# Kernel tuning notes

Hardware: AMD Instinct MI355X
Metric: run time of the kernel (lower is better)

The kernel has to match this reference:

```python
import jax, jax.numpy as jnp
import numpy as np

B_SZ, L, D_MODEL = 2, 1024, 1024
D_INNER, D_STATE, D_CONV = 2048, 16, 4
EPS = 1e-6


def setup_inputs() -> dict:
    key = jax.random.key(0)
    ks = jax.random.split(key, 8)
    def n(k, shape, scale=0.02):
        return jax.random.normal(k, shape, jnp.float32) * scale
    return {
        "x": jax.random.normal(ks[0], (B_SZ, L, D_MODEL), jnp.float32),
        "W_in": n(ks[1], (D_MODEL, 2 * D_INNER)),
        "b_in": jnp.zeros((2 * D_INNER,), jnp.float32),
        "conv_w": n(ks[2], (D_INNER, 1, D_CONV), 0.2),
        "conv_b": jnp.zeros((D_INNER,), jnp.float32),
        "W_xp": n(ks[3], (D_INNER, 2 * D_STATE)),
        "b_xp": jnp.zeros((2 * D_STATE,), jnp.float32),
        "W_dt": n(ks[4], (D_INNER, D_INNER)),
        "b_dt": jnp.full((D_INNER,), -1.0, jnp.float32),
        # torch code does log(randn) (NaN-prone); use log of positive uniform instead
        "A_log": jnp.log(jax.random.uniform(ks[5], (D_INNER, D_STATE), jnp.float32, 0.5, 1.5)),
        "D_skip": jnp.ones((D_INNER,), jnp.float32),
        "W_out": n(ks[6], (D_INNER, D_MODEL)),
        "b_out": jnp.zeros((D_MODEL,), jnp.float32),
        "alpha": jnp.ones((D_MODEL,), jnp.float32),
        "beta": jnp.zeros((D_MODEL,), jnp.float32),
    }


def _selective_scan(xc, delta, A, Bm, Cm, D_skip):
    # xc, delta: (B,L,di); A: (di,ds); Bm, Cm: (B,L,ds)
    dA = jnp.exp(delta[..., None] * A)                     # (B,L,di,ds)
    dBx = (delta * xc)[..., None] * Bm[:, :, None, :]      # (B,L,di,ds)
    h0 = jnp.zeros((xc.shape[0], xc.shape[2], A.shape[1]), xc.dtype)

    def step(h, inp):
        dA_t, dBx_t, C_t = inp
        h = dA_t * h + dBx_t                               # (B,di,ds)
        y_t = jnp.einsum('bds,bs->bd', h, C_t)
        return h, y_t

    _, ys = jax.lax.scan(
        step, h0,
        (dA.transpose(1, 0, 2, 3), dBx.transpose(1, 0, 2, 3), Cm.transpose(1, 0, 2)))
    y = ys.transpose(1, 0, 2)                              # (B,L,di)
    return y + D_skip * xc


def _layernorm(r, alpha, beta):
    # torch LayerNormalization: unbiased std, eps added to std
    mean = jnp.mean(r, axis=-1, keepdims=True)
    diff = r - mean
    var_unb = jnp.sum(diff * diff, axis=-1, keepdims=True) / (r.shape[-1] - 1)
    std = jnp.sqrt(var_unb)
    return alpha * diff / (std + EPS) + beta


def reference(x, W_in, b_in, conv_w, conv_b, W_xp, b_xp, W_dt, b_dt,
              A_log, D_skip, W_out, b_out, alpha, beta):
    residual = x
    xz = x @ W_in + b_in                                   # (B,L,2*di)
    x_in, z = jnp.split(xz, 2, axis=-1)

    # depthwise causal conv1d (torch pads d_conv-1 both sides, slices [:L])
    xt = x_in.transpose(0, 2, 1)                           # (B,di,L)
    xt = jax.lax.conv_general_dilated(
        xt, conv_w, window_strides=(1,), padding=[(D_CONV - 1, 0)],
        feature_group_count=D_INNER, dimension_numbers=('NCH', 'OIH', 'NCH'))
    xt = xt + conv_b[None, :, None]
    x_conv = jax.nn.silu(xt.transpose(0, 2, 1))            # (B,L,di)

    x_proj_out = x_conv @ W_xp + b_xp                      # (B,L,2*ds)
    Bm, Cm = jnp.split(x_proj_out, 2, axis=-1)
    delta = jax.nn.softplus(x_conv @ W_dt + b_dt)          # (B,L,di)
    A = -jnp.exp(A_log)

    y = _selective_scan(x_conv, delta, A, Bm, Cm, D_skip)
    y = y * jax.nn.silu(z)
    out = y @ W_out + b_out                                # (B,L,D)
    return _layernorm(residual + out, alpha, beta)
```

## Files before the change

kernel.cpp:

```cpp
#include <hip/hip_runtime.h>
#include <math.h>

#define B_SZ    2
#define L_SEQ   1024
#define DMODEL  1024
#define DINNER  2048
#define DSTATE  16
#define EPSV    1e-6f

#define CCH 64
#define CS  (L_SEQ / CCH)
#define DT  16
#define SSTR (CCH * DT + 1)

typedef short  bf16x8  __attribute__((ext_vector_type(8)));
typedef float  floatx4 __attribute__((ext_vector_type(4)));
typedef unsigned short ushort8v __attribute__((ext_vector_type(8)));

extern "C" __device__ float __ocml_native_exp2_f32(float);
extern "C" __device__ float __ocml_native_log2_f32(float);

__device__ __forceinline__ float nexp2(float x) { return __ocml_native_exp2_f32(x); }

__device__ __forceinline__ float softplus_f(float v) {
    if (v > 20.f) return v;
    return 0.69314718f * __ocml_native_log2_f32(1.f + nexp2(v * 1.44269504f));
}
__device__ __forceinline__ float silu_f(float z) {
    return z / (1.f + nexp2(z * -1.44269504f));
}

__device__ __forceinline__ unsigned short f2bf(float f) {
    unsigned int u = __float_as_uint(f);
    unsigned int r = (u + 0x7FFFu + ((u >> 16) & 1u)) >> 16;
    return (unsigned short)r;
}
__device__ __forceinline__ float bf2f(unsigned short u) {
    return __uint_as_float(((unsigned int)u) << 16);
}

__global__ __launch_bounds__(256) void cast_bf16_kernel(
    const float* __restrict__ in, unsigned short* __restrict__ out, int n4)
{
    int i = blockIdx.x * 256 + threadIdx.x;
    if (i >= n4) return;
    float4 v = ((const float4*)in)[i];
    ushort4 o = { f2bf(v.x), f2bf(v.y), f2bf(v.z), f2bf(v.w) };
    ((ushort4*)out)[i] = o;
}

__global__ __launch_bounds__(256) void transpose_cast3(
    const float* __restrict__ W_in, unsigned short* __restrict__ W_in_t,
    const float* __restrict__ W_dt, unsigned short* __restrict__ W_dt_t,
    const float* __restrict__ W_out, unsigned short* __restrict__ W_out_t)
{
    __shared__ float tile[32][33];
    const int bid = blockIdx.x;
    const float* W; unsigned short* Wt; int K, N, t;
    if (bid < 4096)      { W = W_in;  Wt = W_in_t;  K = 1024; N = 4096; t = bid; }
    else if (bid < 8192) { W = W_dt;  Wt = W_dt_t;  K = 2048; N = 2048; t = bid - 4096; }
    else                 { W = W_out; Wt = W_out_t; K = 2048; N = 1024; t = bid - 8192; }
    const int nx = N >> 5;
    const int n0 = (t % nx) * 32;
    const int k0 = (t / nx) * 32;
    const int c = threadIdx.x & 31;
    const int r = threadIdx.x >> 5;
#pragma unroll
    for (int i = 0; i < 4; ++i)
        tile[r + 8 * i][c] = W[(size_t)(k0 + r + 8 * i) * N + n0 + c];
    __syncthreads();
#pragma unroll
    for (int i = 0; i < 4; ++i)
        Wt[(size_t)(n0 + r + 8 * i) * K + k0 + c] = f2bf(tile[c][r + 8 * i]);
}

template <int TM, int TN, int MODE>
__global__ __launch_bounds__(256, 2) void gemm_bf16(
    const unsigned short* __restrict__ A, const unsigned short* __restrict__ Bt,
    const float* __restrict__ bias, const float* __restrict__ resid,
    float* __restrict__ C, int M, int N, int K)
{
    constexpr int MI = TM / 32;
    constexpr int NJ = TN / 32;
    constexpr int NLOAD = (TM + TN) / 32;

    __shared__ unsigned short As[TM * 64];
    __shared__ unsigned short Bs[TN * 64];

    const int tid  = threadIdx.x;
    const int wave = tid >> 6;
    const int lane = tid & 63;
    const int m0 = blockIdx.y * TM;
    const int n0 = blockIdx.x * TN;
    const int wm = (wave >> 1) * (TM / 2);
    const int wn = (wave & 1) * (TN / 2);
    const int fr = lane & 15;
    const int kg = lane >> 4;

    int offs[NLOAD];
    unsigned short* lp[NLOAD];
#pragma unroll
    for (int i = 0; i < NLOAD; ++i) {
        const int slot = i * 256 + tid;
        const int row  = slot >> 3;
        const int ch   = slot & 7;
        const int pos  = ch ^ (row & 7);
        if (i < TM / 32) {
            offs[i] = (m0 + row) * K + ch * 8;
            lp[i]   = &As[row * 64 + pos * 8];
        } else {
            const int rb = row - TM;
            offs[i] = (n0 + rb) * K + ch * 8;
            lp[i]   = &Bs[rb * 64 + pos * 8];
        }
    }

    floatx4 acc[MI][NJ] = {};
    bf16x8 pre[NLOAD];

#pragma unroll
    for (int i = 0; i < NLOAD; ++i)
        pre[i] = *(const bf16x8*)((i < TM / 32 ? A : Bt) + offs[i]);
#pragma unroll
    for (int i = 0; i < NLOAD; ++i)
        *(bf16x8*)lp[i] = pre[i];
    __syncthreads();

    for (int kt = 0; kt < K; kt += 64) {
        const bool more = (kt + 64) < K;
        if (more) {
#pragma unroll
            for (int i = 0; i < NLOAD; ++i)
                pre[i] = *(const bf16x8*)((i < TM / 32 ? A : Bt) + offs[i] + kt + 64);
        }

#pragma unroll
        for (int ks = 0; ks < 2; ++ks) {
            const int cq = (ks << 2) | kg;
            bf16x8 af[MI], bfv[NJ];
#pragma unroll
            for (int i = 0; i < MI; ++i) {
                const int row = wm + i * 16 + fr;
                af[i] = *(const bf16x8*)&As[row * 64 + ((cq ^ (row & 7)) << 3)];
            }
#pragma unroll
            for (int j = 0; j < NJ; ++j) {
                const int row = wn + j * 16 + fr;
                bfv[j] = *(const bf16x8*)&Bs[row * 64 + ((cq ^ (row & 7)) << 3)];
            }
#pragma unroll
            for (int i = 0; i < MI; ++i)
#pragma unroll
                for (int j = 0; j < NJ; ++j)
                    acc[i][j] = __builtin_amdgcn_mfma_f32_16x16x32_bf16(
                        af[i], bfv[j], acc[i][j], 0, 0, 0);
        }
        __syncthreads();
        if (more) {
#pragma unroll
            for (int i = 0; i < NLOAD; ++i)
                *(bf16x8*)lp[i] = pre[i];
        }
        __syncthreads();
    }

    const int rq = (lane >> 4) * 4;
    if (MODE == 4) {
        unsigned short* Ct = (unsigned short*)C;
#pragma unroll
        for (int i = 0; i < MI; ++i) {
#pragma unroll
            for (int j = 0; j < NJ; ++j) {
                const int col = n0 + wn + j * 16 + fr;
                const float bv = bias[col];
                const int row0 = m0 + wm + i * 16 + rq;
                ushort4 o;
#pragma unroll
                for (int r = 0; r < 4; ++r)
                    (&o.x)[r] = f2bf(softplus_f(acc[i][j][r] + bv));
                *(ushort4*)&Ct[(size_t)col * M + row0] = o;
            }
        }
    } else {
#pragma unroll
        for (int i = 0; i < MI; ++i) {
#pragma unroll
            for (int j = 0; j < NJ; ++j) {
                const int col = n0 + wn + j * 16 + fr;
                const float bv = bias[col];
#pragma unroll
                for (int r = 0; r < 4; ++r) {
                    const int row = m0 + wm + i * 16 + rq + r;
                    float v = acc[i][j][r] + bv;
                    if (MODE == 1) {
                        v = softplus_f(v);
                    } else if (MODE == 2) {
                        v += resid[(size_t)row * N + col];
                    }
                    C[(size_t)row * N + col] = v;
                }
            }
        }
    }
}

#define CROWS 4
__global__ __launch_bounds__(256) void conv_xproj(
    const float* __restrict__ xz, const float* __restrict__ conv_w,
    const float* __restrict__ conv_b, const float* __restrict__ W_xp,
    const float* __restrict__ b_xp,
    unsigned short* __restrict__ x_conv_bf, float* __restrict__ BC)
{
    __shared__ float sxc[CROWS][DINNER];
    __shared__ float red[8][CROWS][32];

    const int tid = threadIdx.x;
    const int r0 = blockIdx.x * CROWS;
    const int c8 = tid * 8;

    float wt[8][4];
#pragma unroll
    for (int ci = 0; ci < 8; ++ci) {
        float4 w4 = *(const float4*)&conv_w[(c8 + ci) * 4];
        wt[ci][0] = w4.x; wt[ci][1] = w4.y; wt[ci][2] = w4.z; wt[ci][3] = w4.w;
    }
    float cb[8];
    *(float4*)&cb[0] = *(const float4*)&conv_b[c8];
    *(float4*)&cb[4] = *(const float4*)&conv_b[c8 + 4];

#pragma unroll
    for (int rr = 0; rr < CROWS; ++rr) {
        const int row = r0 + rr;
        const int l = row & (L_SEQ - 1);
        float acc[8];
#pragma unroll
        for (int ci = 0; ci < 8; ++ci) acc[ci] = cb[ci];
#pragma unroll
        for (int h = 0; h < 4; ++h) {
            const int lsrc = l - 3 + h;
            if (lsrc >= 0) {
                float4 a = *(const float4*)&xz[(size_t)(row - 3 + h) * (2 * DINNER) + c8];
                float4 b = *(const float4*)&xz[(size_t)(row - 3 + h) * (2 * DINNER) + c8 + 4];
                acc[0] += a.x * wt[0][h]; acc[1] += a.y * wt[1][h];
                acc[2] += a.z * wt[2][h]; acc[3] += a.w * wt[3][h];
                acc[4] += b.x * wt[4][h]; acc[5] += b.y * wt[5][h];
                acc[6] += b.z * wt[6][h]; acc[7] += b.w * wt[7][h];
            }
        }
        float o[8];
        ushort8v ob;
#pragma unroll
        for (int ci = 0; ci < 8; ++ci) {
            o[ci] = silu_f(acc[ci]);
            sxc[rr][c8 + ci] = o[ci];
            ob[ci] = (short)f2bf(o[ci]);
        }
        *(ushort8v*)&x_conv_bf[(size_t)row * DINNER + c8] = ob;
    }
    __syncthreads();

    const int n = tid & 31;
    const int g = tid >> 5;
    float p[CROWS] = {};
    const int k0 = g * 256;
#pragma unroll 4
    for (int k = k0; k < k0 + 256; ++k) {
        const float wv = W_xp[k * 32 + n];
        p[0] += sxc[0][k] * wv;
        p[1] += sxc[1][k] * wv;
        p[2] += sxc[2][k] * wv;
        p[3] += sxc[3][k] * wv;
    }
#pragma unroll
    for (int rr = 0; rr < CROWS; ++rr) red[g][rr][n] = p[rr];
    __syncthreads();
    if (tid < CROWS * 32) {
        const int rr = tid >> 5;
        const int n2 = tid & 31;
        float s = b_xp[n2];
#pragma unroll
        for (int gg = 0; gg < 8; ++gg) s += red[gg][rr][n2];
        BC[(size_t)(r0 + rr) * 32 + n2] = s;
    }
}

__global__ __launch_bounds__(1024) void scan_kernel(
    const unsigned short* __restrict__ deltaT,
    const unsigned short* __restrict__ xc_bf,
    const float* __restrict__ BC, const float* __restrict__ A_log,
    const float* __restrict__ D_skip, const float* __restrict__ xz,
    unsigned short* __restrict__ y_bf)
{
    __shared__ float sA[DSTATE * SSTR];
    __shared__ float sH[DSTATE * SSTR];

    const int tid = threadIdx.x;
    const int dl  = tid & (DT - 1);
    const int c   = tid >> 4;
    const int b   = blockIdx.x >> 7;
    const int d0  = (blockIdx.x & 127) * DT;
    const int d   = d0 + dl;

    float Al[DSTATE];
#pragma unroll
    for (int s = 0; s < DSTATE; ++s)
        Al[s] = -__expf(A_log[d * DSTATE + s]) * 1.44269504f;
    const float Dsk = D_skip[d];

    const int l0 = c * CS;
    const int row0 = b * L_SEQ + l0;

    const unsigned short* dpt = deltaT + (size_t)d * (B_SZ * L_SEQ) + row0;
    bf16x8 dv0 = *(const bf16x8*)dpt;
    bf16x8 dv1 = *(const bf16x8*)(dpt + 8);
    float dts[CS];
    float dsum = 0.f;
#pragma unroll
    for (int k = 0; k < 8; ++k) {
        dts[k]     = bf2f((unsigned short)dv0[k]);
        dts[8 + k] = bf2f((unsigned short)dv1[k]);
    }
#pragma unroll
    for (int k = 0; k < CS; ++k) dsum += dts[k];

    float h[DSTATE];
#pragma unroll
    for (int s = 0; s < DSTATE; ++s) h[s] = 0.f;

    const unsigned short* xcp = xc_bf + (size_t)row0 * DINNER + d;
    const float* bcp = BC + (size_t)row0 * 32;

#pragma unroll 4
    for (int j = 0; j < CS; ++j) {
        const float dt = dts[j];
        const float xc = bf2f(xcp[j * DINNER]);
        float Bv[DSTATE];
        *(float4*)&Bv[0]  = *(const float4*)(bcp + j * 32 + 0);
        *(float4*)&Bv[4]  = *(const float4*)(bcp + j * 32 + 4);
        *(float4*)&Bv[8]  = *(const float4*)(bcp + j * 32 + 8);
        *(float4*)&Bv[12] = *(const float4*)(bcp + j * 32 + 12);
        const float dlx = dt * xc;
#pragma unroll
        for (int s = 0; s < DSTATE; ++s) {
            const float e = nexp2(dt * Al[s]);
            h[s] = e * h[s] + dlx * Bv[s];
        }
    }
#pragma unroll
    for (int s = 0; s < DSTATE; ++s) {
        sH[s * SSTR + c * DT + dl] = h[s];
        sA[s * SSTR + c * DT + dl] = nexp2(Al[s] * dsum);
    }
    __syncthreads();

    if (tid < DSTATE * DT) {
        const int dl2 = tid & (DT - 1);
        const int s2  = tid >> 4;
        float hh = 0.f;
#pragma unroll
        for (int c2 = 0; c2 < CCH; ++c2) {
            const int idx = s2 * SSTR + c2 * DT + dl2;
            const float a  = sA[idx];
            const float he = sH[idx];
            sH[idx] = hh;
            hh = a * hh + he;
        }
    }
    __syncthreads();

#pragma unroll
    for (int s = 0; s < DSTATE; ++s) h[s] = sH[s * SSTR + c * DT + dl];

    const float* zp = xz + (size_t)row0 * (2 * DINNER) + DINNER + d;
    unsigned short* yp = y_bf + (size_t)row0 * DINNER + d;
#pragma unroll 4
    for (int j = 0; j < CS; ++j) {
        const float dt = dts[j];
        const float xc = bf2f(xcp[j * DINNER]);
        const float z  = zp[j * (2 * DINNER)];
        float Bv[DSTATE], Cv[DSTATE];
        *(float4*)&Bv[0]  = *(const float4*)(bcp + j * 32 + 0);
        *(float4*)&Bv[4]  = *(const float4*)(bcp + j * 32 + 4);
        *(float4*)&Bv[8]  = *(const float4*)(bcp + j * 32 + 8);
        *(float4*)&Bv[12] = *(const float4*)(bcp + j * 32 + 12);
        *(float4*)&Cv[0]  = *(const float4*)(bcp + j * 32 + 16);
        *(float4*)&Cv[4]  = *(const float4*)(bcp + j * 32 + 20);
        *(float4*)&Cv[8]  = *(const float4*)(bcp + j * 32 + 24);
        *(float4*)&Cv[12] = *(const float4*)(bcp + j * 32 + 28);
        const float dlx = dt * xc;
        float y = Dsk * xc;
#pragma unroll
        for (int s = 0; s < DSTATE; ++s) {
            const float e = nexp2(dt * Al[s]);
            h[s] = e * h[s] + dlx * Bv[s];
            y += h[s] * Cv[s];
        }
        yp[j * DINNER] = f2bf(y * silu_f(z));
    }
}

__global__ __launch_bounds__(256) void layernorm_kernel(
    const float* __restrict__ t, const float* __restrict__ alpha,
    const float* __restrict__ beta, float* __restrict__ out)
{
    __shared__ float sred[4];
    __shared__ float sred2[4];
    const int row = blockIdx.x;
    const int tid = threadIdx.x;
    const float* r = t + (size_t)row * DMODEL;

    float4 v = *(const float4*)&r[tid * 4];
    float lsum = v.x + v.y + v.z + v.w;
#pragma unroll
    for (int m = 1; m < 64; m <<= 1) lsum += __shfl_xor(lsum, m);
    if ((tid & 63) == 0) sred[tid >> 6] = lsum;
    __syncthreads();
    const float mean = (sred[0] + sred[1] + sred[2] + sred[3]) * (1.f / DMODEL);

    const float dx = v.x - mean, dy = v.y - mean, dz = v.z - mean, dw = v.w - mean;
    float ls2 = dx * dx + dy * dy + dz * dz + dw * dw;
#pragma unroll
    for (int m = 1; m < 64; m <<= 1) ls2 += __shfl_xor(ls2, m);
    if ((tid & 63) == 0) sred2[tid >> 6] = ls2;
    __syncthreads();
    const float var = (sred2[0] + sred2[1] + sred2[2] + sred2[3]) * (1.f / (DMODEL - 1));
    const float inv = 1.f / (sqrtf(var) + EPSV);

    float4 a4 = *(const float4*)&alpha[tid * 4];
    float4 b4 = *(const float4*)&beta[tid * 4];
    float4 o;
    o.x = a4.x * dx * inv + b4.x;
    o.y = a4.y * dy * inv + b4.y;
    o.z = a4.z * dz * inv + b4.z;
    o.w = a4.w * dw * inv + b4.w;
    *(float4*)&out[(size_t)row * DMODEL + tid * 4] = o;
}

extern "C" void kernel_launch(void* const* d_in, const int* in_sizes, int n_in,
                              void* d_out, int out_size, void* d_ws, size_t ws_size,
                              hipStream_t stream)
{
    const float* x      = (const float*)d_in[0];
    const float* W_in   = (const float*)d_in[1];
    const float* b_in   = (const float*)d_in[2];
    const float* conv_w = (const float*)d_in[3];
    const float* conv_b = (const float*)d_in[4];
    const float* W_xp   = (const float*)d_in[5];
    const float* b_xp   = (const float*)d_in[6];
    const float* W_dt   = (const float*)d_in[7];
    const float* b_dt   = (const float*)d_in[8];
    const float* A_log  = (const float*)d_in[9];
    const float* D_skip = (const float*)d_in[10];
    const float* W_out  = (const float*)d_in[11];
    const float* b_out  = (const float*)d_in[12];
    const float* alpha  = (const float*)d_in[13];
    const float* beta   = (const float*)d_in[14];
    float* out = (float*)d_out;

    const size_t M = (size_t)B_SZ * L_SEQ;
    char* ws = (char*)d_ws;
    float* xz      = (float*)(ws + 0);
    unsigned short* deltaT = (unsigned short*)(ws + (48u << 20));
    float* BC      = (float*)(ws + (64u << 20));
    unsigned short* x_bf       = (unsigned short*)(ws + (64u << 20) + (512u << 10));
    unsigned short* W_in_t     = (unsigned short*)(ws + (69u << 20));
    unsigned short* W_dt_t     = (unsigned short*)(ws + (77u << 20));
    unsigned short* W_out_t    = (unsigned short*)(ws + (85u << 20));
    unsigned short* x_conv_bf  = (unsigned short*)(ws + (89u << 20));
    unsigned short* ygate_bf   = (unsigned short*)(ws + (77u << 20));
    float* tpre = xz;

    const dim3 blk(256);

    cast_bf16_kernel<<<dim3((unsigned)(M * DMODEL / 4 / 256)), blk, 0, stream>>>(
        x, x_bf, (int)(M * DMODEL / 4));
    transpose_cast3<<<dim3(10240), blk, 0, stream>>>(
        W_in, W_in_t, W_dt, W_dt_t, W_out, W_out_t);

    gemm_bf16<128, 128, 0><<<dim3(4096 / 128, 2048 / 128), blk, 0, stream>>>(
        x_bf, W_in_t, b_in, nullptr, xz, 2048, 4096, 1024);

    conv_xproj<<<dim3((unsigned)(M / CROWS)), blk, 0, stream>>>(
        xz, conv_w, conv_b, W_xp, b_xp, x_conv_bf, BC);

    gemm_bf16<128, 128, 4><<<dim3(2048 / 128, 2048 / 128), blk, 0, stream>>>(
        x_conv_bf, W_dt_t, b_dt, nullptr, (float*)deltaT, 2048, 2048, 2048);

    scan_kernel<<<dim3(B_SZ * (DINNER / DT)), dim3(1024), 0, stream>>>(
        deltaT, x_conv_bf, BC, A_log, D_skip, xz, ygate_bf);

    gemm_bf16<64, 64, 2><<<dim3(1024 / 64, 2048 / 64), blk, 0, stream>>>(
        ygate_bf, W_out_t, b_out, x, tpre, 2048, 1024, 2048);

    layernorm_kernel<<<dim3((unsigned)M), blk, 0, stream>>>(tpre, alpha, beta, out);
}
```

Measured before the change: 267.9 us.

## Merge prep kernels, tune GEMM tiles and occupancy, store scan carries in bf16

Folds the x cast and the weight transpose-cast into one prep kernel, saving a launch. Retiles the delta GEMM to 128x64 and adds a min-waves template parameter so the delta and output GEMMs request higher occupancy. The scan kernel keeps its chunk carries and decay products in bf16 shared memory instead of fp32 and asks for more blocks per CU, trading accuracy of the cross-chunk state propagation for less LDS per block.

```diff
diff --git a/kernel.cpp b/kernel.cpp
--- a/kernel.cpp
+++ b/kernel.cpp
@@ -11,7 +11,7 @@
 #define CCH 64
 #define CS  (L_SEQ / CCH)
 #define DT  16
-#define SSTR (CCH * DT + 1)
+#define SSTR2 (CCH * DT + 2)
 
 typedef short  bf16x8  __attribute__((ext_vector_type(8)));
 typedef float  floatx4 __attribute__((ext_vector_type(4)));
@@ -39,23 +39,21 @@
     return __uint_as_float(((unsigned int)u) << 16);
 }
 
-__global__ __launch_bounds__(256) void cast_bf16_kernel(
-    const float* __restrict__ in, unsigned short* __restrict__ out, int n4)
-{
-    int i = blockIdx.x * 256 + threadIdx.x;
-    if (i >= n4) return;
-    float4 v = ((const float4*)in)[i];
-    ushort4 o = { f2bf(v.x), f2bf(v.y), f2bf(v.z), f2bf(v.w) };
-    ((ushort4*)out)[i] = o;
-}
-
-__global__ __launch_bounds__(256) void transpose_cast3(
+__global__ __launch_bounds__(256) void prep_kernel(
+    const float* __restrict__ x, unsigned short* __restrict__ x_bf,
     const float* __restrict__ W_in, unsigned short* __restrict__ W_in_t,
     const float* __restrict__ W_dt, unsigned short* __restrict__ W_dt_t,
     const float* __restrict__ W_out, unsigned short* __restrict__ W_out_t)
 {
+    const int bid = blockIdx.x;
+    if (bid >= 10240) {
+        const int i = (bid - 10240) * 256 + threadIdx.x;
+        float4 v = ((const float4*)x)[i];
+        ushort4 o = { f2bf(v.x), f2bf(v.y), f2bf(v.z), f2bf(v.w) };
+        ((ushort4*)x_bf)[i] = o;
+        return;
+    }
     __shared__ float tile[32][33];
-    const int bid = blockIdx.x;
     const float* W; unsigned short* Wt; int K, N, t;
     if (bid < 4096)      { W = W_in;  Wt = W_in_t;  K = 1024; N = 4096; t = bid; }
     else if (bid < 8192) { W = W_dt;  Wt = W_dt_t;  K = 2048; N = 2048; t = bid - 4096; }
@@ -74,8 +72,8 @@
         Wt[(size_t)(n0 + r + 8 * i) * K + k0 + c] = f2bf(tile[c][r + 8 * i]);
 }
 
-template <int TM, int TN, int MODE>
-__global__ __launch_bounds__(256, 2) void gemm_bf16(
+template <int TM, int TN, int MODE, int MINW>
+__global__ __launch_bounds__(256, MINW) void gemm_bf16(
     const unsigned short* __restrict__ A, const unsigned short* __restrict__ Bt,
     const float* __restrict__ bias, const float* __restrict__ resid,
     float* __restrict__ C, int M, int N, int K)
@@ -284,15 +282,15 @@
     }
 }
 
-__global__ __launch_bounds__(1024) void scan_kernel(
+__global__ __launch_bounds__(1024, 8) void scan_kernel(
     const unsigned short* __restrict__ deltaT,
     const unsigned short* __restrict__ xc_bf,
     const float* __restrict__ BC, const float* __restrict__ A_log,
     const float* __restrict__ D_skip, const float* __restrict__ xz,
     unsigned short* __restrict__ y_bf)
 {
-    __shared__ float sA[DSTATE * SSTR];
-    __shared__ float sH[DSTATE * SSTR];
+    __shared__ unsigned short sA[DSTATE * SSTR2];
+    __shared__ unsigned short sH[DSTATE * SSTR2];
 
     const int tid = threadIdx.x;
     const int dl  = tid & (DT - 1);
@@ -348,8 +346,8 @@
     }
 #pragma unroll
     for (int s = 0; s < DSTATE; ++s) {
-        sH[s * SSTR + c * DT + dl] = h[s];
-        sA[s * SSTR + c * DT + dl] = nexp2(Al[s] * dsum);
+        sH[s * SSTR2 + c * DT + dl] = f2bf(h[s]);
+        sA[s * SSTR2 + c * DT + dl] = f2bf(nexp2(Al[s] * dsum));
     }
     __syncthreads();
 
@@ -359,17 +357,17 @@
         float hh = 0.f;
 #pragma unroll
         for (int c2 = 0; c2 < CCH; ++c2) {
-            const int idx = s2 * SSTR + c2 * DT + dl2;
-            const float a  = sA[idx];
-            const float he = sH[idx];
-            sH[idx] = hh;
+            const int idx = s2 * SSTR2 + c2 * DT + dl2;
+            const float a  = bf2f(sA[idx]);
+            const float he = bf2f(sH[idx]);
+            sH[idx] = f2bf(hh);
             hh = a * hh + he;
         }
     }
     __syncthreads();
 
 #pragma unroll
-    for (int s = 0; s < DSTATE; ++s) h[s] = sH[s * SSTR + c * DT + dl];
+    for (int s = 0; s < DSTATE; ++s) h[s] = bf2f(sH[s * SSTR2 + c * DT + dl]);
 
     const float* zp = xz + (size_t)row0 * (2 * DINNER) + DINNER + d;
     unsigned short* yp = y_bf + (size_t)row0 * DINNER + d;
@@ -472,24 +470,22 @@
 
     const dim3 blk(256);
 
-    cast_bf16_kernel<<<dim3((unsigned)(M * DMODEL / 4 / 256)), blk, 0, stream>>>(
-        x, x_bf, (int)(M * DMODEL / 4));
-    transpose_cast3<<<dim3(10240), blk, 0, stream>>>(
-        W_in, W_in_t, W_dt, W_dt_t, W_out, W_out_t);
-
-    gemm_bf16<128, 128, 0><<<dim3(4096 / 128, 2048 / 128), blk, 0, stream>>>(
+    prep_kernel<<<dim3(12288), blk, 0, stream>>>(
+        x, x_bf, W_in, W_in_t, W_dt, W_dt_t, W_out, W_out_t);
+
+    gemm_bf16<128, 128, 0, 2><<<dim3(4096 / 128, 2048 / 128), blk, 0, stream>>>(
         x_bf, W_in_t, b_in, nullptr, xz, 2048, 4096, 1024);
 
     conv_xproj<<<dim3((unsigned)(M / CROWS)), blk, 0, stream>>>(
         xz, conv_w, conv_b, W_xp, b_xp, x_conv_bf, BC);
 
-    gemm_bf16<128, 128, 4><<<dim3(2048 / 128, 2048 / 128), blk, 0, stream>>>(
+    gemm_bf16<128, 64, 4, 3><<<dim3(2048 / 64, 2048 / 128), blk, 0, stream>>>(
         x_conv_bf, W_dt_t, b_dt, nullptr, (float*)deltaT, 2048, 2048, 2048);
 
     scan_kernel<<<dim3(B_SZ * (DINNER / DT)), dim3(1024), 0, stream>>>(
         deltaT, x_conv_bf, BC, A_log, D_skip, xz, ygate_bf);
 
-    gemm_bf16<64, 64, 2><<<dim3(1024 / 64, 2048 / 64), blk, 0, stream>>>(
+    gemm_bf16<64, 64, 2, 3><<<dim3(1024 / 64, 2048 / 64), blk, 0, stream>>>(
         ygate_bf, W_out_t, b_out, x, tpre, 2048, 1024, 2048);
 
     layernorm_kernel<<<dim3((unsigned)M), blk, 0, stream>>>(tpre, alpha, beta, out);
```

After: 364.7 us. 36.1% more time.
